# Kernel optimization log

Hardware: AMD Instinct MI355X
Metric: run time of the kernel (lower is better)

The kernel has to match this reference:

```python
import jax, jax.numpy as jnp
import numpy as np

BS, N_AGENTS, SA_DIM, HID = 2048, 64, 128, 256


def setup_inputs() -> dict:
    key = jax.random.key(0)
    ks = jax.random.split(key, 16)
    s = lambda fan_in: 1.0 / np.sqrt(fan_in)
    u = lambda k, shp, b: jax.random.uniform(k, shp, jnp.float32, -b, b)
    return {
        "x": jax.random.normal(ks[0], (BS, N_AGENTS, SA_DIM), jnp.float32),
        # encoder: Linear(sa, hid) -> Linear(hid, hid)
        "enc_w1": u(ks[1], (SA_DIM, HID), s(SA_DIM)),
        "enc_b1": u(ks[2], (HID,), s(SA_DIM)),
        "enc_w2": u(ks[3], (HID, HID), s(HID)),
        "enc_b2": u(ks[4], (HID,), s(HID)),
        # attention 'general' linear_in (no bias)
        "attn_w": u(ks[5], (HID, HID), s(HID)),
        # gc1: Linear(sa, hid); nn_gc1: Linear(sa, hid)
        "gc1_w": u(ks[6], (SA_DIM, HID), s(SA_DIM)),
        "gc1_b": u(ks[7], (HID,), s(SA_DIM)),
        "nn1_w": u(ks[8], (SA_DIM, HID), s(SA_DIM)),
        "nn1_b": u(ks[9], (HID,), s(SA_DIM)),
        # gc2: Linear(hid, hid); nn_gc2: Linear(hid, hid)
        "gc2_w": u(ks[10], (HID, HID), s(HID)),
        "gc2_b": u(ks[11], (HID,), s(HID)),
        "nn2_w": u(ks[12], (HID, HID), s(HID)),
        "nn2_b": u(ks[13], (HID,), s(HID)),
        "n_agents": N_AGENTS,
    }


def reference(x, enc_w1, enc_b1, enc_w2, enc_b2, attn_w,
              gc1_w, gc1_b, nn1_w, nn1_b, gc2_w, gc2_b, nn2_w, nn2_b,
              n_agents):
    relu = jax.nn.relu
    inv_n = 1.0 / n_agents
    # encoder MLP: relu(relu(x W1 + b1) W2 + b2)  -> [bs, n, hid]
    emb = relu(relu(x @ enc_w1 + enc_b1) @ enc_w2 + enc_b2)
    # general attention: softmax((emb W_a) emb^T) over last axis -> [bs, n, n]
    scores = jnp.einsum('bnd,bmd->bnm', emb @ attn_w, emb)
    attn = jax.nn.softmax(scores, axis=-1)
    # gc1: adj @ Linear(x); residual relu branch; normalize by n_agents
    feat = relu(jnp.einsum('bnm,bmh->bnh', attn, x @ gc1_w + gc1_b))
    feat = (feat + relu(x @ nn1_w + nn1_b)) * inv_n
    # gc2 on feat
    out = relu(jnp.einsum('bnm,bmh->bnh', attn, feat @ gc2_w + gc2_b))
    out = (out + relu(feat @ nn2_w + nn2_b)) * inv_n
    return out, attn
```

## Files before the change

kernel.cpp:

```cpp
#include <hip/hip_runtime.h>

typedef _Float16 half8 __attribute__((ext_vector_type(8)));
typedef _Float16 half4_t __attribute__((ext_vector_type(4)));
typedef float f32x4 __attribute__((ext_vector_type(4)));

#define NBATCH 2048
#define NA 64
#define SA 128
#define HID 256

#define OFF_R0 0
#define OFF_ATT 16384
#define SMEM_BYTES 40960

#define W_ENC1 0
#define W_ENC2 (W_ENC1 + 128 * 256)
#define W_ATTN (W_ENC2 + 256 * 256)
#define W_GC1 (W_ATTN + 256 * 256)
#define W_NN1 (W_GC1 + 128 * 256)
#define W_GC2 (W_NN1 + 128 * 256)
#define W_NN2 (W_GC2 + 256 * 256)

#define MFMA(a, b, cacc) __builtin_amdgcn_mfma_f32_16x16x32_f16((a), (b), (cacc), 0, 0, 0)

__global__ void pack_all(const float* __restrict__ e1, const float* __restrict__ e2,
                         const float* __restrict__ aw, const float* __restrict__ g1,
                         const float* __restrict__ n1, const float* __restrict__ g2,
                         const float* __restrict__ n2, _Float16* __restrict__ dst) {
  int b = (int)blockIdx.x;
  const float* src;
  int off;
  if (b < 16) { src = e1; off = W_ENC1; }
  else if (b < 48) { src = e2; off = W_ENC2; b -= 16; }
  else if (b < 80) { src = aw; off = W_ATTN; b -= 48; }
  else if (b < 96) { src = g1; off = W_GC1; b -= 80; }
  else if (b < 112) { src = n1; off = W_NN1; b -= 96; }
  else if (b < 144) { src = g2; off = W_GC2; b -= 112; }
  else { src = n2; off = W_NN2; b -= 144; }
  int t = b * 256 + (int)threadIdx.x;
  int lane = t & 63, frag = t >> 6;
  int nt = frag & 15, kt = frag >> 4;
  int g = lane >> 4, c = lane & 15;
  half8 h;
#pragma unroll
  for (int j = 0; j < 8; ++j)
    h[j] = (_Float16)src[(size_t)(kt * 32 + g * 8 + j) * 256 + nt * 16 + c];
  *(half8*)(dst + off + (size_t)t * 8) = h;
}

__global__ __launch_bounds__(256, 2) void dicg_main(
    const float* __restrict__ x, const float* __restrict__ b_enc1,
    const float* __restrict__ b_enc2, const float* __restrict__ b_gc1,
    const float* __restrict__ b_nn1, const float* __restrict__ b_gc2,
    const float* __restrict__ b_nn2, const _Float16* __restrict__ wp,
    float* __restrict__ out, float* __restrict__ attn_out) {
  extern __shared__ _Float16 sm[];
  _Float16* R0 = sm + OFF_R0;
  _Float16* ATTp = sm + OFF_ATT;

  const int tid = (int)threadIdx.x;
  const int wv = tid >> 6;
  const int lane = tid & 63;
  const int g = lane >> 4;
  const int c = lane & 15;
  const int bb = (int)blockIdx.x;
  const float* __restrict__ xb = x + (size_t)bb * (NA * SA);

  auto ldA = [&](const _Float16* p, int kt, int rt) -> half8 {
    return *(const half8*)(p + (kt * 4 + rt) * 512 + lane * 8);
  };
  auto ldB = [&](const _Float16* p, int kt, int ct) -> half8 {
    return *(const half8*)(p + (kt * 16 + ct) * 512 + lane * 8);
  };
  auto wfrag = [&](const _Float16* wb, int kt, int ntg) -> half8 {
    return *(const half8*)(wb + ((size_t)(kt * 16 + ntg) * 64 + lane) * 8);
  };
  auto xfrag = [&](int r0, int k0) -> half8 {
    const float* p = xb + (r0 + c) * SA + k0 + g * 8;
    f32x4 u = *(const f32x4*)p;
    f32x4 v = *(const f32x4*)(p + 4);
    half8 h;
    h[0] = (_Float16)u[0]; h[1] = (_Float16)u[1];
    h[2] = (_Float16)u[2]; h[3] = (_Float16)u[3];
    h[4] = (_Float16)v[0]; h[5] = (_Float16)v[1];
    h[6] = (_Float16)v[2]; h[7] = (_Float16)v[3];
    return h;
  };

  auto stA_val = [&](_Float16* dst, int rt, int nt, int r, float v) {
    int kt = 2 * wv + (nt >> 1);
    int lanep = (2 * (nt & 1) + (c >> 3)) * 16 + 4 * g + r;
    dst[(kt * 4 + rt) * 512 + lanep * 8 + (c & 7)] = (_Float16)v;
  };
  auto ep_storeA = [&](f32x4(&acc)[4][4], const float* bias, bool dorelu) {
#pragma unroll
    for (int nt = 0; nt < 4; ++nt) {
      float bv = bias[64 * wv + 16 * nt + c];
#pragma unroll
      for (int rt = 0; rt < 4; ++rt)
#pragma unroll
        for (int r = 0; r < 4; ++r) {
          float y = acc[rt][nt][r] + bv;
          if (dorelu) y = fmaxf(y, 0.f);
          stA_val(R0, rt, nt, r, y);
        }
    }
  };
  auto ep_storeB = [&](f32x4(&acc)[4][4], const float* bias) {
#pragma unroll
    for (int nt = 0; nt < 4; ++nt) {
      float bv = bias[64 * wv + 16 * nt + c];
#pragma unroll
      for (int rt = 0; rt < 4; ++rt) {
        half4_t h;
#pragma unroll
        for (int r = 0; r < 4; ++r) h[r] = (_Float16)(acc[rt][nt][r] + bv);
        int fi = (rt >> 1) * 16 + 4 * wv + nt;
        int lanep = (2 * (rt & 1) + (g >> 1)) * 16 + c;
        *(half4_t*)(R0 + fi * 512 + lanep * 8 + 4 * (g & 1)) = h;
      }
    }
  };
  auto stQ = [&](const f32x4(&q2)[2], int s) {
    _Float16* base = ATTp + (wv + 4 * s) * 512;
#pragma unroll
    for (int nt2 = 0; nt2 < 2; ++nt2)
#pragma unroll
      for (int r = 0; r < 4; ++r)
        base[((2 * nt2 + (c >> 3)) * 16 + 4 * g + r) * 8 + (c & 7)] = (_Float16)q2[nt2][r];
  };

  auto mmA = [&](f32x4(&acc)[4][4], const _Float16* Ap, const _Float16* wb, int nkt) {
#pragma unroll
    for (int kt = 0; kt < nkt; ++kt) {
      half8 af[4], bf[4];
#pragma unroll
      for (int rt = 0; rt < 4; ++rt) af[rt] = ldA(Ap, kt, rt);
#pragma unroll
      for (int nt = 0; nt < 4; ++nt) bf[nt] = wfrag(wb, kt, 4 * wv + nt);
#pragma unroll
      for (int rt = 0; rt < 4; ++rt)
#pragma unroll
        for (int nt = 0; nt < 4; ++nt) acc[rt][nt] = MFMA(af[rt], bf[nt], acc[rt][nt]);
    }
  };
  auto mm_x = [&](f32x4(&acc)[4][4], const _Float16* wb) {
#pragma unroll
    for (int kt = 0; kt < 4; ++kt) {
      half8 af[4], bf[4];
#pragma unroll
      for (int rt = 0; rt < 4; ++rt) af[rt] = xfrag(16 * rt, kt * 32);
#pragma unroll
      for (int nt = 0; nt < 4; ++nt) bf[nt] = wfrag(wb, kt, 4 * wv + nt);
#pragma unroll
      for (int rt = 0; rt < 4; ++rt)
#pragma unroll
        for (int nt = 0; nt < 4; ++nt) acc[rt][nt] = MFMA(af[rt], bf[nt], acc[rt][nt]);
    }
  };
  auto mm_x2 = [&](f32x4(&a1)[4][4], f32x4(&a2)[4][4], const _Float16* wb1,
                   const _Float16* wb2) {
#pragma unroll
    for (int kt = 0; kt < 4; ++kt) {
      half8 af[4], b1[4], b2[4];
#pragma unroll
      for (int rt = 0; rt < 4; ++rt) af[rt] = xfrag(16 * rt, kt * 32);
#pragma unroll
      for (int nt = 0; nt < 4; ++nt) b1[nt] = wfrag(wb1, kt, 4 * wv + nt);
#pragma unroll
      for (int nt = 0; nt < 4; ++nt) b2[nt] = wfrag(wb2, kt, 4 * wv + nt);
#pragma unroll
      for (int rt = 0; rt < 4; ++rt)
#pragma unroll
        for (int nt = 0; nt < 4; ++nt) {
          a1[rt][nt] = MFMA(af[rt], b1[nt], a1[rt][nt]);
          a2[rt][nt] = MFMA(af[rt], b2[nt], a2[rt][nt]);
        }
    }
  };
  auto mmA2 = [&](f32x4(&a1)[4][4], f32x4(&a2)[4][4], const _Float16* Ap,
                  const _Float16* wb1, const _Float16* wb2, int nkt) {
#pragma unroll
    for (int kt = 0; kt < nkt; ++kt) {
      half8 af[4], b1[4], b2[4];
#pragma unroll
      for (int rt = 0; rt < 4; ++rt) af[rt] = ldA(Ap, kt, rt);
#pragma unroll
      for (int nt = 0; nt < 4; ++nt) b1[nt] = wfrag(wb1, kt, 4 * wv + nt);
#pragma unroll
      for (int nt = 0; nt < 4; ++nt) b2[nt] = wfrag(wb2, kt, 4 * wv + nt);
#pragma unroll
      for (int rt = 0; rt < 4; ++rt)
#pragma unroll
        for (int nt = 0; nt < 4; ++nt) {
          a1[rt][nt] = MFMA(af[rt], b1[nt], a1[rt][nt]);
          a2[rt][nt] = MFMA(af[rt], b2[nt], a2[rt][nt]);
        }
    }
  };
  auto mm_att = [&](f32x4(&acc)[4][4]) {
#pragma unroll
    for (int kt = 0; kt < 2; ++kt) {
      half8 af[4], bf[4];
#pragma unroll
      for (int rt = 0; rt < 4; ++rt) af[rt] = ldA(ATTp, kt, rt);
#pragma unroll
      for (int nt = 0; nt < 4; ++nt) bf[nt] = ldB(R0, kt, 4 * wv + nt);
#pragma unroll
      for (int rt = 0; rt < 4; ++rt)
#pragma unroll
        for (int nt = 0; nt < 4; ++nt) acc[rt][nt] = MFMA(af[rt], bf[nt], acc[rt][nt]);
    }
  };

  {
    f32x4 acc[4][4]{};
    mm_x(acc, wp + W_ENC1);
    ep_storeA(acc, b_enc1, true);
  }
  __syncthreads();
  {
    f32x4 acc[4][4]{};
    mmA(acc, R0, wp + W_ENC2, 8);
    __syncthreads();
    ep_storeA(acc, b_enc2, true);
  }
  __syncthreads();
  {
    half8 aeK[8];
#pragma unroll
    for (int k2 = 0; k2 < 8; ++k2) aeK[k2] = ldA(R0, k2, wv);
    f32x4 sc[4]{};
    {
      f32x4 q2[2]{};
#pragma unroll
      for (int k2 = 0; k2 < 8; ++k2) {
        q2[0] = MFMA(aeK[k2], wfrag(wp + W_ATTN, k2, 0), q2[0]);
        q2[1] = MFMA(aeK[k2], wfrag(wp + W_ATTN, k2, 1), q2[1]);
      }
      stQ(q2, 0);
    }
#pragma unroll
    for (int ktp = 0; ktp < 8; ++ktp) {
      f32x4 q2n[2]{};
      if (ktp < 7) {
#pragma unroll
        for (int k2 = 0; k2 < 8; ++k2) {
          q2n[0] = MFMA(aeK[k2], wfrag(wp + W_ATTN, k2, 2 * ktp + 2), q2n[0]);
          q2n[1] = MFMA(aeK[k2], wfrag(wp + W_ATTN, k2, 2 * ktp + 3), q2n[1]);
        }
      }
      asm volatile("s_waitcnt lgkmcnt(0)" ::: "memory");
      half8 qb = *(const half8*)(ATTp + (wv + 4 * (ktp & 1)) * 512 + lane * 8);
      if (ktp < 7) stQ(q2n, (ktp + 1) & 1);
#pragma unroll
      for (int rt = 0; rt < 4; ++rt) sc[rt] = MFMA(ldA(R0, ktp, rt), qb, sc[rt]);
    }
    float m = sc[0][0];
#pragma unroll
    for (int rt = 0; rt < 4; ++rt)
#pragma unroll
      for (int r = 0; r < 4; ++r) m = fmaxf(m, sc[rt][r]);
    m = fmaxf(m, __shfl_xor(m, 16));
    m = fmaxf(m, __shfl_xor(m, 32));
    float e[4][4], s = 0.f;
#pragma unroll
    for (int rt = 0; rt < 4; ++rt)
#pragma unroll
      for (int r = 0; r < 4; ++r) {
        e[rt][r] = __expf(sc[rt][r] - m);
        s += e[rt][r];
      }
    s += __shfl_xor(s, 16);
    s += __shfl_xor(s, 32);
    float inv = 1.0f / s;
    float* ao = attn_out + ((size_t)bb * NA + 16 * wv + c) * NA;
#pragma unroll
    for (int rt = 0; rt < 4; ++rt) {
      f32x4 vv;
      half4_t hh;
#pragma unroll
      for (int r = 0; r < 4; ++r) {
        vv[r] = e[rt][r] * inv;
        hh[r] = (_Float16)vv[r];
      }
      *(f32x4*)(ao + 16 * rt + 4 * g) = vv;
      int fi = (rt >> 1) * 4 + wv;
      int lanep = (2 * (rt & 1) + (g >> 1)) * 16 + c;
      *(half4_t*)(ATTp + fi * 512 + lanep * 8 + 4 * (g & 1)) = hh;
    }
  }
  __syncthreads();
  half4_t r1h[4][4];
  {
    f32x4 aG[4][4]{}, aN[4][4]{};
    mm_x2(aG, aN, wp + W_GC1, wp + W_NN1);
    ep_storeB(aG, b_gc1);
#pragma unroll
    for (int nt = 0; nt < 4; ++nt) {
      float bv = b_nn1[64 * wv + 16 * nt + c];
#pragma unroll
      for (int rt = 0; rt < 4; ++rt)
#pragma unroll
        for (int r = 0; r < 4; ++r)
          r1h[rt][nt][r] = (_Float16)fmaxf(aN[rt][nt][r] + bv, 0.f);
    }
  }
  __syncthreads();
  {
    f32x4 a1[4][4]{};
    mm_att(a1);
    __syncthreads();
#pragma unroll
    for (int nt = 0; nt < 4; ++nt)
#pragma unroll
      for (int rt = 0; rt < 4; ++rt)
#pragma unroll
        for (int r = 0; r < 4; ++r)
          stA_val(R0, rt, nt, r,
                  (fmaxf(a1[rt][nt][r], 0.f) + (float)r1h[rt][nt][r]) * 0.015625f);
  }
  __syncthreads();
  half4_t r2h[4][4];
  {
    f32x4 aN2[4][4]{}, aG2[4][4]{};
    mmA2(aN2, aG2, R0, wp + W_NN2, wp + W_GC2, 8);
#pragma unroll
    for (int nt = 0; nt < 4; ++nt) {
      float bv = b_nn2[64 * wv + 16 * nt + c];
#pragma unroll
      for (int rt = 0; rt < 4; ++rt)
#pragma unroll
        for (int r = 0; r < 4; ++r)
          r2h[rt][nt][r] = (_Float16)fmaxf(aN2[rt][nt][r] + bv, 0.f);
    }
    __syncthreads();
    ep_storeB(aG2, b_gc2);
  }
  __syncthreads();
  {
    f32x4 a1[4][4]{};
    mm_att(a1);
    float* ob = out + (size_t)bb * NA * HID;
#pragma unroll
    for (int nt = 0; nt < 4; ++nt)
#pragma unroll
      for (int rt = 0; rt < 4; ++rt)
#pragma unroll
        for (int r = 0; r < 4; ++r)
          ob[(size_t)(16 * rt + 4 * g + r) * HID + 64 * wv + 16 * nt + c] =
              (fmaxf(a1[rt][nt][r], 0.f) + (float)r2h[rt][nt][r]) * 0.015625f;
  }
}

extern "C" void kernel_launch(void* const* d_in, const int* in_sizes, int n_in,
                              void* d_out, int out_size, void* d_ws, size_t ws_size,
                              hipStream_t stream) {
  const float* x = (const float*)d_in[0];
  const float* enc_w1 = (const float*)d_in[1];
  const float* enc_b1 = (const float*)d_in[2];
  const float* enc_w2 = (const float*)d_in[3];
  const float* enc_b2 = (const float*)d_in[4];
  const float* attn_w = (const float*)d_in[5];
  const float* gc1_w = (const float*)d_in[6];
  const float* gc1_b = (const float*)d_in[7];
  const float* nn1_w = (const float*)d_in[8];
  const float* nn1_b = (const float*)d_in[9];
  const float* gc2_w = (const float*)d_in[10];
  const float* gc2_b = (const float*)d_in[11];
  const float* nn2_w = (const float*)d_in[12];
  const float* nn2_b = (const float*)d_in[13];

  _Float16* wp = (_Float16*)d_ws;
  float* out = (float*)d_out;
  float* attn_o = out + (size_t)NBATCH * NA * HID;

  pack_all<<<176, 256, 0, stream>>>(enc_w1, enc_w2, attn_w, gc1_w, nn1_w, gc2_w,
                                    nn2_w, wp);
  dicg_main<<<NBATCH, 256, SMEM_BYTES, stream>>>(
      x, enc_b1, enc_b2, gc1_b, nn1_b, gc2_b, nn2_b, wp, out, attn_o);
}
```

Baseline: 189.2 us.

## Compute attention projection as full GEMM into double-buffered LDS

Replaces the per-wave interleaved Q-projection/score loop, in which each wave recomputed a slice of emb·W_a, with a full block-wide GEMM that writes emb·W_a to a second LDS buffer. The scores then come from a plain 8-step MFMA loop over the two buffers. Ping-ponging between two buffers also removes a __syncthreads in the encoder stage. LDS use grows from 40 KB to 64 KB per block, which may reduce occupancy below the two blocks per CU requested by the launch bounds.

```diff
diff --git a/kernel.cpp b/kernel.cpp
--- a/kernel.cpp
+++ b/kernel.cpp
@@ -9,9 +9,9 @@
 #define SA 128
 #define HID 256
 
-#define OFF_R0 0
-#define OFF_ATT 16384
-#define SMEM_BYTES 40960
+#define OFF_RA 0
+#define OFF_RB 16384
+#define SMEM_BYTES 65536
 
 #define W_ENC1 0
 #define W_ENC2 (W_ENC1 + 128 * 256)
@@ -55,8 +55,8 @@
     const float* __restrict__ b_nn2, const _Float16* __restrict__ wp,
     float* __restrict__ out, float* __restrict__ attn_out) {
   extern __shared__ _Float16 sm[];
-  _Float16* R0 = sm + OFF_R0;
-  _Float16* ATTp = sm + OFF_ATT;
+  _Float16* RA = sm + OFF_RA;
+  _Float16* RB = sm + OFF_RB;
 
   const int tid = (int)threadIdx.x;
   const int wv = tid >> 6;
@@ -92,21 +92,22 @@
     int lanep = (2 * (nt & 1) + (c >> 3)) * 16 + 4 * g + r;
     dst[(kt * 4 + rt) * 512 + lanep * 8 + (c & 7)] = (_Float16)v;
   };
-  auto ep_storeA = [&](f32x4(&acc)[4][4], const float* bias, bool dorelu) {
+  auto ep_storeA = [&](_Float16* dst, f32x4(&acc)[4][4], const float* bias,
+                       bool dorelu) {
 #pragma unroll
     for (int nt = 0; nt < 4; ++nt) {
-      float bv = bias[64 * wv + 16 * nt + c];
+      float bv = bias ? bias[64 * wv + 16 * nt + c] : 0.f;
 #pragma unroll
       for (int rt = 0; rt < 4; ++rt)
 #pragma unroll
         for (int r = 0; r < 4; ++r) {
           float y = acc[rt][nt][r] + bv;
           if (dorelu) y = fmaxf(y, 0.f);
-          stA_val(R0, rt, nt, r, y);
+          stA_val(dst, rt, nt, r, y);
         }
     }
   };
-  auto ep_storeB = [&](f32x4(&acc)[4][4], const float* bias) {
+  auto ep_storeB = [&](_Float16* dst, f32x4(&acc)[4][4], const float* bias) {
 #pragma unroll
     for (int nt = 0; nt < 4; ++nt) {
       float bv = bias[64 * wv + 16 * nt + c];
@@ -117,17 +118,9 @@
         for (int r = 0; r < 4; ++r) h[r] = (_Float16)(acc[rt][nt][r] + bv);
         int fi = (rt >> 1) * 16 + 4 * wv + nt;
         int lanep = (2 * (rt & 1) + (g >> 1)) * 16 + c;
-        *(half4_t*)(R0 + fi * 512 + lanep * 8 + 4 * (g & 1)) = h;
+        *(half4_t*)(dst + fi * 512 + lanep * 8 + 4 * (g & 1)) = h;
       }
     }
-  };
-  auto stQ = [&](const f32x4(&q2)[2], int s) {
-    _Float16* base = ATTp + (wv + 4 * s) * 512;
-#pragma unroll
-    for (int nt2 = 0; nt2 < 2; ++nt2)
-#pragma unroll
-      for (int r = 0; r < 4; ++r)
-        base[((2 * nt2 + (c >> 3)) * 16 + 4 * g + r) * 8 + (c & 7)] = (_Float16)q2[nt2][r];
   };
 
   auto mmA = [&](f32x4(&acc)[4][4], const _Float16* Ap, const _Float16* wb, int nkt) {
@@ -203,9 +196,9 @@
     for (int kt = 0; kt < 2; ++kt) {
       half8 af[4], bf[4];
 #pragma unroll
-      for (int rt = 0; rt < 4; ++rt) af[rt] = ldA(ATTp, kt, rt);
-#pragma unroll
-      for (int nt = 0; nt < 4; ++nt) bf[nt] = ldB(R0, kt, 4 * wv + nt);
+      for (int rt = 0; rt < 4; ++rt) af[rt] = ldA(RA, kt, rt);
+#pragma unroll
+      for (int nt = 0; nt < 4; ++nt) bf[nt] = ldB(RB, kt, 4 * wv + nt);
 #pragma unroll
       for (int rt = 0; rt < 4; ++rt)
 #pragma unroll
@@ -216,78 +209,61 @@
   {
     f32x4 acc[4][4]{};
     mm_x(acc, wp + W_ENC1);
-    ep_storeA(acc, b_enc1, true);
+    ep_storeA(RA, acc, b_enc1, true);
   }
   __syncthreads();
   {
     f32x4 acc[4][4]{};
-    mmA(acc, R0, wp + W_ENC2, 8);
-    __syncthreads();
-    ep_storeA(acc, b_enc2, true);
-  }
-  __syncthreads();
-  {
-    half8 aeK[8];
-#pragma unroll
-    for (int k2 = 0; k2 < 8; ++k2) aeK[k2] = ldA(R0, k2, wv);
+    mmA(acc, RA, wp + W_ENC2, 8);
+    ep_storeA(RB, acc, b_enc2, true);
+  }
+  __syncthreads();
+  {
+    f32x4 acc[4][4]{};
+    mmA(acc, RB, wp + W_ATTN, 8);
+    ep_storeA(RA, acc, nullptr, false);
+  }
+  __syncthreads();
+  {
     f32x4 sc[4]{};
-    {
-      f32x4 q2[2]{};
-#pragma unroll
-      for (int k2 = 0; k2 < 8; ++k2) {
-        q2[0] = MFMA(aeK[k2], wfrag(wp + W_ATTN, k2, 0), q2[0]);
-        q2[1] = MFMA(aeK[k2], wfrag(wp + W_ATTN, k2, 1), q2[1]);
-      }
-      stQ(q2, 0);
-    }
-#pragma unroll
-    for (int ktp = 0; ktp < 8; ++ktp) {
-      f32x4 q2n[2]{};
-      if (ktp < 7) {
-#pragma unroll
-        for (int k2 = 0; k2 < 8; ++k2) {
-          q2n[0] = MFMA(aeK[k2], wfrag(wp + W_ATTN, k2, 2 * ktp + 2), q2n[0]);
-          q2n[1] = MFMA(aeK[k2], wfrag(wp + W_ATTN, k2, 2 * ktp + 3), q2n[1]);
-        }
-      }
-      asm volatile("s_waitcnt lgkmcnt(0)" ::: "memory");
-      half8 qb = *(const half8*)(ATTp + (wv + 4 * (ktp & 1)) * 512 + lane * 8);
-      if (ktp < 7) stQ(q2n, (ktp + 1) & 1);
-#pragma unroll
-      for (int rt = 0; rt < 4; ++rt) sc[rt] = MFMA(ldA(R0, ktp, rt), qb, sc[rt]);
+#pragma unroll
+    for (int kt = 0; kt < 8; ++kt) {
+      half8 zb = ldA(RA, kt, wv);
+#pragma unroll
+      for (int mt = 0; mt < 4; ++mt) sc[mt] = MFMA(ldA(RB, kt, mt), zb, sc[mt]);
     }
     float m = sc[0][0];
 #pragma unroll
-    for (int rt = 0; rt < 4; ++rt)
-#pragma unroll
-      for (int r = 0; r < 4; ++r) m = fmaxf(m, sc[rt][r]);
+    for (int mt = 0; mt < 4; ++mt)
+#pragma unroll
+      for (int r = 0; r < 4; ++r) m = fmaxf(m, sc[mt][r]);
     m = fmaxf(m, __shfl_xor(m, 16));
     m = fmaxf(m, __shfl_xor(m, 32));
     float e[4][4], s = 0.f;
 #pragma unroll
-    for (int rt = 0; rt < 4; ++rt)
+    for (int mt = 0; mt < 4; ++mt)
 #pragma unroll
       for (int r = 0; r < 4; ++r) {
-        e[rt][r] = __expf(sc[rt][r] - m);
-        s += e[rt][r];
+        e[mt][r] = __expf(sc[mt][r] - m);
+        s += e[mt][r];
       }
     s += __shfl_xor(s, 16);
     s += __shfl_xor(s, 32);
     float inv = 1.0f / s;
     float* ao = attn_out + ((size_t)bb * NA + 16 * wv + c) * NA;
 #pragma unroll
-    for (int rt = 0; rt < 4; ++rt) {
+    for (int mt = 0; mt < 4; ++mt) {
       f32x4 vv;
       half4_t hh;
 #pragma unroll
       for (int r = 0; r < 4; ++r) {
-        vv[r] = e[rt][r] * inv;
+        vv[r] = e[mt][r] * inv;
         hh[r] = (_Float16)vv[r];
       }
-      *(f32x4*)(ao + 16 * rt + 4 * g) = vv;
-      int fi = (rt >> 1) * 4 + wv;
-      int lanep = (2 * (rt & 1) + (g >> 1)) * 16 + c;
-      *(half4_t*)(ATTp + fi * 512 + lanep * 8 + 4 * (g & 1)) = hh;
+      *(f32x4*)(ao + 16 * mt + 4 * g) = vv;
+      int fi = (mt >> 1) * 4 + wv;
+      int lanep = (2 * (mt & 1) + (g >> 1)) * 16 + c;
+      *(half4_t*)(RA + fi * 512 + lanep * 8 + 4 * (g & 1)) = hh;
     }
   }
   __syncthreads();
@@ -295,7 +271,7 @@
   {
     f32x4 aG[4][4]{}, aN[4][4]{};
     mm_x2(aG, aN, wp + W_GC1, wp + W_NN1);
-    ep_storeB(aG, b_gc1);
+    ep_storeB(RB, aG, b_gc1);
 #pragma unroll
     for (int nt = 0; nt < 4; ++nt) {
       float bv = b_nn1[64 * wv + 16 * nt + c];
@@ -317,14 +293,14 @@
       for (int rt = 0; rt < 4; ++rt)
 #pragma unroll
         for (int r = 0; r < 4; ++r)
-          stA_val(R0, rt, nt, r,
+          stA_val(RB, rt, nt, r,
                   (fmaxf(a1[rt][nt][r], 0.f) + (float)r1h[rt][nt][r]) * 0.015625f);
   }
   __syncthreads();
   half4_t r2h[4][4];
   {
     f32x4 aN2[4][4]{}, aG2[4][4]{};
-    mmA2(aN2, aG2, R0, wp + W_NN2, wp + W_GC2, 8);
+    mmA2(aN2, aG2, RB, wp + W_NN2, wp + W_GC2, 8);
 #pragma unroll
     for (int nt = 0; nt < 4; ++nt) {
       float bv = b_nn2[64 * wv + 16 * nt + c];
@@ -335,7 +311,7 @@
           r2h[rt][nt][r] = (_Float16)fmaxf(aN2[rt][nt][r] + bv, 0.f);
     }
     __syncthreads();
-    ep_storeB(aG2, b_gc2);
+    ep_storeB(RB, aG2, b_gc2);
   }
   __syncthreads();
   {
```

Result: slower. 205.7 us (+8.7%).
